# Kernel tuning notes

Hardware: AMD Instinct MI355X
Metric: run time of the kernel (lower is better)

The kernel has to match this reference:

```python
import jax, jax.numpy as jnp
import numpy as np

NUM_HEADS = 12

def setup_inputs() -> dict:
    key = jax.random.key(0)
    ks = jax.random.split(key, 6)
    B, N, C, P = 16, 785, 768, 48
    return {
        "x": jax.random.normal(ks[0], (B, N, C), jnp.float32),
        "qkv_w": jax.random.normal(ks[1], (3 * C, C), jnp.float32) * 0.02,
        "pos_emb": jax.random.normal(ks[2], (N, N, P), jnp.float32) * 0.02,
        "pos_proj_w": jax.random.normal(ks[3], (NUM_HEADS, P), jnp.float32) * 0.02,
        "proj_w": jax.random.normal(ks[4], (C, C), jnp.float32) * 0.02,
        "proj_b": jnp.zeros((C,), jnp.float32),
    }

def reference(x, qkv_w, pos_emb, pos_proj_w, proj_w, proj_b):
    B, N, C = x.shape
    H = NUM_HEADS
    hd = C // H
    scale = hd ** -0.5
    # qkv projection: [B,N,3C] -> q,k,v each [B,H,N,hd]
    qkv = (x @ qkv_w.T).reshape(B, N, 3, H, hd)
    qkv = jnp.transpose(qkv, (2, 0, 3, 1, 4))
    q, k, v = qkv[0], qkv[1], qkv[2]
    # learned relative-position bias: [H,N,N]
    pos_score = jnp.einsum('nmp,hp->hnm', pos_emb, pos_proj_w)
    # attention scores: scale applied AFTER adding bias (matches original)
    attn = (jnp.einsum('bhnd,bhmd->bhnm', q, k) + pos_score[None]) * scale
    attn = jax.nn.softmax(attn, axis=-1)
    out = jnp.einsum('bhnm,bhmd->bhnd', attn, v)
    out = jnp.transpose(out, (0, 2, 1, 3)).reshape(B, N, C)
    return out @ proj_w.T + proj_b
```

## Files before the change

kernel.cpp:

```cpp
#include <hip/hip_runtime.h>
#include <hip/hip_fp16.h>

#define B_ 16
#define N_ 785
#define NP 800
#define C_ 768
#define H_ 12
#define HD_ 64
#define P_ 48
#define M_ (B_*N_)
#define MP_ (B_*NP)
#define POSW 832
#define VTW  832
#define SLOG2E 0.1803368801111244f

#define OFF_Q   0
#define OFF_K   9646080
#define OFF_VT  19292160
#define OFF_POS 29515776
#define OFF_XF  37353216
#define OFF_AO  OFF_XF
#define OFF_WQ  47085312
#define OFF_WP  48854784

struct __align__(16) Half8 { __half h[8]; };
typedef _Float16 half8_t __attribute__((ext_vector_type(8)));
typedef _Float16 half4_t __attribute__((ext_vector_type(4)));
typedef float f32x4 __attribute__((ext_vector_type(4)));

__device__ __forceinline__ void gl16(const void* g, void* l) {
    __builtin_amdgcn_global_load_lds(
        (const __attribute__((address_space(1))) void*)g,
        (__attribute__((address_space(3))) void*)l, 16, 0, 0);
}

__device__ __forceinline__ int xcd_swz(int o, int nwg) {
    const int q = nwg >> 3, r = nwg & 7;
    const int xcd = o & 7, idx = o >> 3;
    const int base = xcd < r ? xcd * (q + 1) : r * (q + 1) + (xcd - r) * q;
    return base + idx;
}

#define NX4 2411520
#define NQ4 442368
#define NP4 147456
#define NTOT4 (NX4+NQ4+NP4)

__global__ __launch_bounds__(256) void convert_f16(
    const float* __restrict__ x, const float* __restrict__ wq,
    const float* __restrict__ wp, _Float16* __restrict__ xo,
    _Float16* __restrict__ wqo, _Float16* __restrict__ wpo)
{
    int i = blockIdx.x * 256 + threadIdx.x;
    const float4* s; _Float16* d; int o;
    if (i < NX4)            { s = (const float4*)x;  d = xo;  o = i; }
    else if (i < NX4 + NQ4) { s = (const float4*)wq; d = wqo; o = i - NX4; }
    else                    { s = (const float4*)wp; d = wpo; o = i - NX4 - NQ4; }
    float4 v = s[o];
    half4_t h = { (_Float16)v.x, (_Float16)v.y, (_Float16)v.z, (_Float16)v.w };
    *(half4_t*)&d[o * 4] = h;
}

#define QKV_NWG (18 * 100)

__global__ __launch_bounds__(256) void qkv_gemm_mfma(
    const _Float16* __restrict__ A, const _Float16* __restrict__ Bw,
    _Float16* __restrict__ qh, _Float16* __restrict__ kh, _Float16* __restrict__ vth)
{
    __shared__ _Float16 Asl[2][128 * 32];
    __shared__ _Float16 Bsl[2][128 * 32];

    const int t  = threadIdx.x;
    const int w  = t >> 6;
    const int l  = t & 63;
    const int lr = l & 15;
    const int lg = l >> 4;
    const int wm = (w >> 1) * 64;
    const int wn = (w & 1) * 64;

    const int g   = xcd_swz(blockIdx.x, QKV_NWG);
    const int nt  = g % 18;
    const int n0  = nt * 128;
    const int mp0 = (g / 18) * 128;
    const int tsel  = nt / 6;
    const bool isV  = (tsel == 2);
    const int nbase = n0 - tsel * 768;

    const int f1 = t + 256;
    const int ar0 = t >> 2,  ac0 = (t & 3) * 8;
    const int ar1 = f1 >> 2, ac1 = (f1 & 3) * 8;
    const int mpa = mp0 + ar0, mpb = mp0 + ar1;
    const int xra = (mpa / NP) * N_ + min(mpa % NP, N_ - 1);
    const int xrb = (mpb / NP) * N_ + min(mpb % NP, N_ - 1);
    const _Float16* Ag0 = A  + (size_t)xra * 768 + ac0;
    const _Float16* Ag1 = A  + (size_t)xrb * 768 + ac1;
    const _Float16* Bg0 = Bw + (size_t)(n0 + ar0) * 768 + ac0;
    const _Float16* Bg1 = Bw + (size_t)(n0 + ar1) * 768 + ac1;

    f32x4 acc[4][4];
    #pragma unroll
    for (int i = 0; i < 4; ++i)
        #pragma unroll
        for (int j = 0; j < 4; ++j) acc[i][j] = (f32x4){0.f, 0.f, 0.f, 0.f};

    gl16(Ag0, &Asl[0][t * 8]); gl16(Ag1, &Asl[0][f1 * 8]);
    gl16(Bg0, &Bsl[0][t * 8]); gl16(Bg1, &Bsl[0][f1 * 8]);
    __syncthreads();

    #pragma unroll 2
    for (int it = 0; it < 24; ++it) {
        const int cur = it & 1;
        if (it < 23) {
            const int kn = (it + 1) * 32;
            gl16(Ag0 + kn, &Asl[cur ^ 1][t * 8]); gl16(Ag1 + kn, &Asl[cur ^ 1][f1 * 8]);
            gl16(Bg0 + kn, &Bsl[cur ^ 1][t * 8]); gl16(Bg1 + kn, &Bsl[cur ^ 1][f1 * 8]);
        }
        half8_t af[4], bf[4];
        #pragma unroll
        for (int i = 0; i < 4; ++i)
            af[i] = *(const half8_t*)&Asl[cur][(wm + i * 16 + lr) * 32 + lg * 8];
        #pragma unroll
        for (int j = 0; j < 4; ++j)
            bf[j] = *(const half8_t*)&Bsl[cur][(wn + j * 16 + lr) * 32 + lg * 8];
        __builtin_amdgcn_s_setprio(1);
        if (!isV) {
            #pragma unroll
            for (int i = 0; i < 4; ++i)
                #pragma unroll
                for (int j = 0; j < 4; ++j)
                    acc[i][j] = __builtin_amdgcn_mfma_f32_16x16x32_f16(bf[j], af[i], acc[i][j], 0, 0, 0);
        } else {
            #pragma unroll
            for (int i = 0; i < 4; ++i)
                #pragma unroll
                for (int j = 0; j < 4; ++j)
                    acc[i][j] = __builtin_amdgcn_mfma_f32_16x16x32_f16(af[i], bf[j], acc[i][j], 0, 0, 0);
        }
        __builtin_amdgcn_s_setprio(0);
        __syncthreads();
    }

    if (!isV) {
        _Float16* dstb = (tsel == 0) ? qh : kh;
        const float sc  = (tsel == 0) ? SLOG2E : 1.0f;
        #pragma unroll
        for (int i = 0; i < 4; ++i) {
            const int mp = mp0 + wm + i * 16 + lr;
            const int bb = mp / NP;
            const int nn = mp - bb * NP;
            if (nn >= N_) continue;
            #pragma unroll
            for (int j = 0; j < 4; ++j) {
                const int nq = nbase + wn + j * 16 + lg * 4;
                const int hh = nq >> 6, dd = nq & 63;
                half4_t hv = { (_Float16)(acc[i][j][0] * sc), (_Float16)(acc[i][j][1] * sc),
                               (_Float16)(acc[i][j][2] * sc), (_Float16)(acc[i][j][3] * sc) };
                *(half4_t*)(dstb + ((size_t)(bb * H_ + hh) * N_ + nn) * HD_ + dd) = hv;
            }
        }
    } else {
        #pragma unroll
        for (int i = 0; i < 4; ++i) {
            const int mq  = mp0 + wm + i * 16 + lg * 4;
            const int bb  = mq / NP;
            const int nn0 = mq - bb * NP;
            if (nn0 >= N_) continue;
            const bool full = (nn0 + 3) < N_;
            #pragma unroll
            for (int j = 0; j < 4; ++j) {
                const int n  = nbase + wn + j * 16 + lr;
                const int hh = n >> 6, dd = n & 63;
                _Float16* vb = vth + ((size_t)(bb * H_ + hh) * HD_ + dd) * VTW;
                if (full) {
                    half4_t hv = { (_Float16)acc[i][j][0], (_Float16)acc[i][j][1],
                                   (_Float16)acc[i][j][2], (_Float16)acc[i][j][3] };
                    *(half4_t*)(vb + nn0) = hv;
                } else {
                    #pragma unroll
                    for (int r = 0; r < 4; ++r)
                        if (nn0 + r < N_) vb[nn0 + r] = (_Float16)acc[i][j][r];
                }
            }
        }
    }
}

__global__ __launch_bounds__(256) void pos_kernel(
    const float* __restrict__ pe, const float* __restrict__ pw,
    __half* __restrict__ posh)
{
    __shared__ float W[H_][P_];
    const int t = threadIdx.x;
    for (int i = t; i < H_ * P_; i += 256) W[i / P_][i % P_] = pw[i];
    __syncthreads();
    int nm = blockIdx.x * 256 + t;
    if (nm >= N_ * N_) return;
    float e[48];
    const float4* src = (const float4*)(pe + (size_t)nm * 48);
    #pragma unroll
    for (int i = 0; i < 12; ++i) {
        float4 v = src[i];
        e[4*i] = v.x; e[4*i+1] = v.y; e[4*i+2] = v.z; e[4*i+3] = v.w;
    }
    int n = nm / N_, m = nm - n * N_;
    #pragma unroll
    for (int hh = 0; hh < H_; ++hh) {
        float s = 0.f;
        #pragma unroll
        for (int p = 0; p < 48; ++p) s = fmaf(e[p], W[hh][p], s);
        posh[((size_t)hh * N_ + n) * POSW + m] = __float2half(s * SLOG2E);
    }
}

#define NQT 13
#define ATT_NWG (192 * NQT)

__global__ __launch_bounds__(256) void attn_mfma(
    const _Float16* __restrict__ qh, const _Float16* __restrict__ kh,
    const _Float16* __restrict__ vt, const _Float16* __restrict__ posh,
    _Float16* __restrict__ aoh)
{
    __shared__ _Float16 Kl[64][72];
    __shared__ _Float16 Vl[64][72];

    const int t  = threadIdx.x;
    const int w  = t >> 6;
    const int l  = t & 63;
    const int lr = l & 15;
    const int lg = l >> 4;

    const int g2   = xcd_swz(blockIdx.x, ATT_NWG);
    const int qt   = g2 % NQT;
    const int rest = g2 / NQT;
    const int b    = rest & 15;
    const int h    = rest >> 4;
    const int bh   = b * H_ + h;
    const int n0   = qt * 64;

    const int qrow = n0 + w * 16 + lr;
    const int qrc  = qrow < N_ ? qrow : N_ - 1;
    const _Float16* qbase = qh + ((size_t)bh * N_ + qrc) * HD_;
    const half8_t qf0 = *(const half8_t*)(qbase + lg * 8);
    const half8_t qf1 = *(const half8_t*)(qbase + 32 + lg * 8);

    f32x4 O0 = {0.f,0.f,0.f,0.f}, O1 = O0, O2 = O0, O3 = O0;
    float m_run = -1e30f;
    float l_lane = 0.f;

    const int srow = t >> 2;
    const int scol = (t & 3) * 16;
    const _Float16* kRow = kh + ((size_t)bh * N_) * HD_ + scol;
    const _Float16* vRow = vt + ((size_t)bh * HD_ + srow) * VTW + scol;
    const _Float16* bFrag = posh + ((size_t)h * N_ + qrc) * POSW + lg * 4;

    half8_t rk0, rk1, rv0, rv1;
    half4_t rbc[4], rbn[4];
    {
        const int gm = srow < N_ ? srow : N_ - 1;
        const half8_t* ks = (const half8_t*)(kRow + (size_t)gm * HD_);
        rk0 = ks[0]; rk1 = ks[1];
        const half8_t* vs = (const half8_t*)vRow;
        rv0 = vs[0]; rv1 = vs[1];
        #pragma unroll
        for (int ms = 0; ms < 4; ++ms)
            rbc[ms] = *(const half4_t*)(bFrag + ms * 16);
    }

    for (int c = 0; c < 13; ++c) {
        *(half8_t*)&Kl[srow][scol]     = rk0;
        *(half8_t*)&Kl[srow][scol + 8] = rk1;
        *(half8_t*)&Vl[srow][scol]     = rv0;
        *(half8_t*)&Vl[srow][scol + 8] = rv1;
        __syncthreads();

        if (c < 12) {
            const int m0n = (c + 1) * 64;
            const int gm  = (m0n + srow) < N_ ? (m0n + srow) : N_ - 1;
            const half8_t* ks = (const half8_t*)(kRow + (size_t)gm * HD_);
            rk0 = ks[0]; rk1 = ks[1];
            const half8_t* vs = (const half8_t*)(vRow + m0n);
            rv0 = vs[0]; rv1 = vs[1];
            #pragma unroll
            for (int ms = 0; ms < 4; ++ms)
                rbn[ms] = *(const half4_t*)(bFrag + m0n + ms * 16);
        }

        f32x4 s[4];
        __builtin_amdgcn_s_setprio(1);
        #pragma unroll
        for (int ms = 0; ms < 4; ++ms) {
            f32x4 acc = { (float)rbc[ms][0], (float)rbc[ms][1],
                          (float)rbc[ms][2], (float)rbc[ms][3] };
            half8_t k0 = *(const half8_t*)&Kl[ms * 16 + lr][lg * 8];
            half8_t k1 = *(const half8_t*)&Kl[ms * 16 + lr][32 + lg * 8];
            acc = __builtin_amdgcn_mfma_f32_16x16x32_f16(k0, qf0, acc, 0, 0, 0);
            acc = __builtin_amdgcn_mfma_f32_16x16x32_f16(k1, qf1, acc, 0, 0, 0);
            s[ms] = acc;
        }
        __builtin_amdgcn_s_setprio(0);

        if (c == 12) {
            #pragma unroll
            for (int ms = 0; ms < 4; ++ms)
                #pragma unroll
                for (int r = 0; r < 4; ++r)
                    if (ms * 16 + lg * 4 + r >= 17) s[ms][r] = -1e30f;
        }

        float x0 = fmaxf(fmaxf(s[0][0], s[0][1]), s[0][2]);
        float x1 = fmaxf(fmaxf(s[0][3], s[1][0]), s[1][1]);
        float x2 = fmaxf(fmaxf(s[1][2], s[1][3]), s[2][0]);
        float x3 = fmaxf(fmaxf(s[2][1], s[2][2]), s[2][3]);
        float x4 = fmaxf(fmaxf(s[3][0], s[3][1]), s[3][2]);
        float smax = fmaxf(fmaxf(fmaxf(x0, x1), x2),
                           fmaxf(fmaxf(x3, x4), s[3][3]));
        smax = fmaxf(smax, __shfl_xor(smax, 16));
        smax = fmaxf(smax, __shfl_xor(smax, 32));

        if (__any(smax > m_run + 8.f)) {
            const float mn    = fmaxf(m_run, smax);
            const float alpha = exp2f(m_run - mn);
            m_run = mn;
            l_lane *= alpha;
            const float a0 = __shfl(alpha, lg * 4 + 0);
            const float a1 = __shfl(alpha, lg * 4 + 1);
            const float a2 = __shfl(alpha, lg * 4 + 2);
            const float a3 = __shfl(alpha, lg * 4 + 3);
            O0[0]*=a0; O0[1]*=a1; O0[2]*=a2; O0[3]*=a3;
            O1[0]*=a0; O1[1]*=a1; O1[2]*=a2; O1[3]*=a3;
            O2[0]*=a0; O2[1]*=a1; O2[2]*=a2; O2[3]*=a3;
            O3[0]*=a0; O3[1]*=a1; O3[2]*=a2; O3[3]*=a3;
        }

        float p[4][4];
        float psum = 0.f;
        #pragma unroll
        for (int ms = 0; ms < 4; ++ms)
            #pragma unroll
            for (int r = 0; r < 4; ++r) {
                p[ms][r] = exp2f(s[ms][r] - m_run);
                psum += p[ms][r];
            }
        l_lane += psum;

        half8_t pa0 = { (_Float16)p[0][0], (_Float16)p[0][1], (_Float16)p[0][2], (_Float16)p[0][3],
                        (_Float16)p[1][0], (_Float16)p[1][1], (_Float16)p[1][2], (_Float16)p[1][3] };
        half8_t pa1 = { (_Float16)p[2][0], (_Float16)p[2][1], (_Float16)p[2][2], (_Float16)p[2][3],
                        (_Float16)p[3][0], (_Float16)p[3][1], (_Float16)p[3][2], (_Float16)p[3][3] };

        __builtin_amdgcn_s_setprio(1);
        #pragma unroll
        for (int ds = 0; ds < 4; ++ds) {
            const _Float16* vr = &Vl[ds * 16 + lr][0];
            half4_t v00 = *(const half4_t*)&vr[lg * 4];
            half4_t v01 = *(const half4_t*)&vr[16 + lg * 4];
            half4_t v10 = *(const half4_t*)&vr[32 + lg * 4];
            half4_t v11 = *(const half4_t*)&vr[48 + lg * 4];
            half8_t vf0 = __builtin_shufflevector(v00, v01, 0, 1, 2, 3, 4, 5, 6, 7);
            half8_t vf1 = __builtin_shufflevector(v10, v11, 0, 1, 2, 3, 4, 5, 6, 7);
            f32x4& Od = (ds == 0 ? O0 : ds == 1 ? O1 : ds == 2 ? O2 : O3);
            Od = __builtin_amdgcn_mfma_f32_16x16x32_f16(pa0, vf0, Od, 0, 0, 0);
            Od = __builtin_amdgcn_mfma_f32_16x16x32_f16(pa1, vf1, Od, 0, 0, 0);
        }
        __builtin_amdgcn_s_setprio(0);
        __syncthreads();

        #pragma unroll
        for (int ms = 0; ms < 4; ++ms) rbc[ms] = rbn[ms];
    }

    float l_row = l_lane;
    l_row += __shfl_xor(l_row, 16);
    l_row += __shfl_xor(l_row, 32);
    const int bb = bh / H_;
    #pragma unroll
    for (int r = 0; r < 4; ++r) {
        const int n = n0 + w * 16 + lg * 4 + r;
        if (n >= N_) continue;
        const float lv  = __shfl(l_row, lg * 4 + r);
        const float inv = 1.f / lv;
        _Float16* dst = aoh + ((size_t)(bb * N_ + n)) * C_ + h * HD_;
        dst[0 * 16 + lr] = (_Float16)(O0[r] * inv);
        dst[1 * 16 + lr] = (_Float16)(O1[r] * inv);
        dst[2 * 16 + lr] = (_Float16)(O2[r] * inv);
        dst[3 * 16 + lr] = (_Float16)(O3[r] * inv);
    }
}

#define PROJ_NWG (6 * 99)

__global__ __launch_bounds__(256) void proj_gemm_mfma(
    const _Float16* __restrict__ A, const _Float16* __restrict__ Bw,
    const float* __restrict__ bias, float* __restrict__ out)
{
    __shared__ _Float16 Asl[2][128 * 32];
    __shared__ _Float16 Bsl[2][128 * 32];

    const int t  = threadIdx.x;
    const int w  = t >> 6;
    const int l  = t & 63;
    const int lr = l & 15;
    const int lg = l >> 4;
    const int wm = (w >> 1) * 64;
    const int wn = (w & 1) * 64;

    const int g  = xcd_swz(blockIdx.x, PROJ_NWG);
    const int n0 = (g % 6) * 128;
    const int m0 = (g / 6) * 128;

    const int f1 = t + 256;
    const int ar0 = t >> 2,  ac0 = (t & 3) * 8;
    const int ar1 = f1 >> 2, ac1 = (f1 & 3) * 8;
    const int ma0 = min(m0 + ar0, M_ - 1);
    const int ma1 = min(m0 + ar1, M_ - 1);
    const _Float16* Ag0 = A  + (size_t)ma0 * 768 + ac0;
    const _Float16* Ag1 = A  + (size_t)ma1 * 768 + ac1;
    const _Float16* Bg0 = Bw + (size_t)(n0 + ar0) * 768 + ac0;
    const _Float16* Bg1 = Bw + (size_t)(n0 + ar1) * 768 + ac1;

    f32x4 acc[4][4];
    #pragma unroll
    for (int i = 0; i < 4; ++i)
        #pragma unroll
        for (int j = 0; j < 4; ++j) acc[i][j] = (f32x4){0.f, 0.f, 0.f, 0.f};

    gl16(Ag0, &Asl[0][t * 8]); gl16(Ag1, &Asl[0][f1 * 8]);
    gl16(Bg0, &Bsl[0][t * 8]); gl16(Bg1, &Bsl[0][f1 * 8]);
    __syncthreads();

    #pragma unroll 2
    for (int it = 0; it < 24; ++it) {
        const int cur = it & 1;
        if (it < 23) {
            const int kn = (it + 1) * 32;
            gl16(Ag0 + kn, &Asl[cur ^ 1][t * 8]); gl16(Ag1 + kn, &Asl[cur ^ 1][f1 * 8]);
            gl16(Bg0 + kn, &Bsl[cur ^ 1][t * 8]); gl16(Bg1 + kn, &Bsl[cur ^ 1][f1 * 8]);
        }
        half8_t af[4], bf[4];
        #pragma unroll
        for (int i = 0; i < 4; ++i)
            af[i] = *(const half8_t*)&Asl[cur][(wm + i * 16 + lr) * 32 + lg * 8];
        #pragma unroll
        for (int j = 0; j < 4; ++j)
            bf[j] = *(const half8_t*)&Bsl[cur][(wn + j * 16 + lr) * 32 + lg * 8];
        __builtin_amdgcn_s_setprio(1);
        #pragma unroll
        for (int i = 0; i < 4; ++i)
            #pragma unroll
            for (int j = 0; j < 4; ++j)
                acc[i][j] = __builtin_amdgcn_mfma_f32_16x16x32_f16(bf[j], af[i], acc[i][j], 0, 0, 0);
        __builtin_amdgcn_s_setprio(0);
        __syncthreads();
    }

    float4 bj4[4];
    #pragma unroll
    for (int j = 0; j < 4; ++j)
        bj4[j] = *(const float4*)&bias[n0 + wn + j * 16 + lg * 4];
    #pragma unroll
    for (int i = 0; i < 4; ++i) {
        const int m = m0 + wm + i * 16 + lr;
        if (m >= M_) continue;
        #pragma unroll
        for (int j = 0; j < 4; ++j) {
            const int nq = n0 + wn + j * 16 + lg * 4;
            float4 o = { acc[i][j][0] + bj4[j].x, acc[i][j][1] + bj4[j].y,
                         acc[i][j][2] + bj4[j].z, acc[i][j][3] + bj4[j].w };
            *(float4*)&out[(size_t)m * 768 + nq] = o;
        }
    }
}

extern "C" void kernel_launch(void* const* d_in, const int* in_sizes, int n_in,
                              void* d_out, int out_size, void* d_ws, size_t ws_size,
                              hipStream_t stream)
{
    const float* x     = (const float*)d_in[0];
    const float* qkv_w = (const float*)d_in[1];
    const float* pe    = (const float*)d_in[2];
    const float* pw    = (const float*)d_in[3];
    const float* pjw   = (const float*)d_in[4];
    const float* pjb   = (const float*)d_in[5];
    float* out = (float*)d_out;

    _Float16* wsh  = (_Float16*)d_ws;
    _Float16* qh   = wsh + OFF_Q;
    _Float16* kh   = wsh + OFF_K;
    _Float16* vth  = wsh + OFF_VT;
    _Float16* posh = wsh + OFF_POS;
    _Float16* xf   = wsh + OFF_XF;
    _Float16* aoh  = wsh + OFF_AO;
    _Float16* wqf  = wsh + OFF_WQ;
    _Float16* wpf  = wsh + OFF_WP;

    convert_f16<<<dim3(NTOT4 / 256), 256, 0, stream>>>(x, qkv_w, pjw, xf, wqf, wpf);
    qkv_gemm_mfma<<<dim3(QKV_NWG), 256, 0, stream>>>(xf, wqf, qh, kh, vth);
    pos_kernel<<<dim3((N_ * N_ + 255) / 256), 256, 0, stream>>>(pe, pw, (__half*)posh);
    attn_mfma<<<dim3(ATT_NWG), 256, 0, stream>>>(qh, kh, vth, posh, aoh);
    proj_gemm_mfma<<<dim3(PROJ_NWG), 256, 0, stream>>>(aoh, wpf, pjb, out);
}
```

Before: 263.5 us.

## Double-buffer K/V LDS tiles and compute softmax row sums via MFMA

Makes the K and V shared-memory tiles double-buffered, so the next chunk is written to the alternate buffer after the PV MFMAs. This removes one of the two block barriers per iteration. V is permuted on store so each lane reads its B fragment with a single 8-wide LDS load instead of two 4-wide loads plus a shuffle. The softmax denominator is accumulated by an extra pair of MFMAs against a vector of ones, replacing scalar adds and the final cross-lane reductions. The max reduction shuffles now run only when a rescale is triggered. Costs are doubled LDS usage, which may lower occupancy, and two extra MFMAs per chunk.

New measurement: 261.6 us. About the same (-0.7%).

```diff
diff --git a/kernel.cpp b/kernel.cpp
--- a/kernel.cpp
+++ b/kernel.cpp
@@ -220,12 +220,12 @@
     const _Float16* __restrict__ vt, const _Float16* __restrict__ posh,
     _Float16* __restrict__ aoh)
 {
-    __shared__ _Float16 Kl[64][72];
-    __shared__ _Float16 Vl[64][72];
+    __shared__ _Float16 Kl[2][64][72];
+    __shared__ _Float16 Vl[2][64][72];
 
     const int t  = threadIdx.x;
+    const int l  = t & 63;
     const int w  = t >> 6;
-    const int l  = t & 63;
     const int lr = l & 15;
     const int lg = l >> 4;
 
@@ -244,11 +244,15 @@
     const half8_t qf1 = *(const half8_t*)(qbase + 32 + lg * 8);
 
     f32x4 O0 = {0.f,0.f,0.f,0.f}, O1 = O0, O2 = O0, O3 = O0;
+    f32x4 lacc = {0.f,0.f,0.f,0.f};
     float m_run = -1e30f;
-    float l_lane = 0.f;
+
+    const half8_t vones = { (_Float16)1.f, (_Float16)1.f, (_Float16)1.f, (_Float16)1.f,
+                            (_Float16)1.f, (_Float16)1.f, (_Float16)1.f, (_Float16)1.f };
 
     const int srow = t >> 2;
     const int scol = (t & 3) * 16;
+    const int vbase = (scol & 32) + ((scol & 16) >> 2);
     const _Float16* kRow = kh + ((size_t)bh * N_) * HD_ + scol;
     const _Float16* vRow = vt + ((size_t)bh * HD_ + srow) * VTW + scol;
     const _Float16* bFrag = posh + ((size_t)h * N_ + qrc) * POSW + lg * 4;
@@ -265,12 +269,18 @@
         for (int ms = 0; ms < 4; ++ms)
             rbc[ms] = *(const half4_t*)(bFrag + ms * 16);
     }
+    *(half8_t*)&Kl[0][srow][scol]     = rk0;
+    *(half8_t*)&Kl[0][srow][scol + 8] = rk1;
+    {
+        _Float16* vd = &Vl[0][srow][vbase];
+        *(half4_t*)(vd +  0) = __builtin_shufflevector(rv0, rv0, 0, 1, 2, 3);
+        *(half4_t*)(vd +  8) = __builtin_shufflevector(rv0, rv0, 4, 5, 6, 7);
+        *(half4_t*)(vd + 16) = __builtin_shufflevector(rv1, rv1, 0, 1, 2, 3);
+        *(half4_t*)(vd + 24) = __builtin_shufflevector(rv1, rv1, 4, 5, 6, 7);
+    }
 
     for (int c = 0; c < 13; ++c) {
-        *(half8_t*)&Kl[srow][scol]     = rk0;
-        *(half8_t*)&Kl[srow][scol + 8] = rk1;
-        *(half8_t*)&Vl[srow][scol]     = rv0;
-        *(half8_t*)&Vl[srow][scol + 8] = rv1;
+        const int cur = c & 1;
         __syncthreads();
 
         if (c < 12) {
@@ -291,8 +301,8 @@
         for (int ms = 0; ms < 4; ++ms) {
             f32x4 acc = { (float)rbc[ms][0], (float)rbc[ms][1],
                           (float)rbc[ms][2], (float)rbc[ms][3] };
-            half8_t k0 = *(const half8_t*)&Kl[ms * 16 + lr][lg * 8];
-            half8_t k1 = *(const half8_t*)&Kl[ms * 16 + lr][32 + lg * 8];
+            half8_t k0 = *(const half8_t*)&Kl[cur][ms * 16 + lr][lg * 8];
+            half8_t k1 = *(const half8_t*)&Kl[cur][ms * 16 + lr][32 + lg * 8];
             acc = __builtin_amdgcn_mfma_f32_16x16x32_f16(k0, qf0, acc, 0, 0, 0);
             acc = __builtin_amdgcn_mfma_f32_16x16x32_f16(k1, qf1, acc, 0, 0, 0);
             s[ms] = acc;
@@ -312,16 +322,15 @@
         float x2 = fmaxf(fmaxf(s[1][2], s[1][3]), s[2][0]);
         float x3 = fmaxf(fmaxf(s[2][1], s[2][2]), s[2][3]);
         float x4 = fmaxf(fmaxf(s[3][0], s[3][1]), s[3][2]);
-        float smax = fmaxf(fmaxf(fmaxf(x0, x1), x2),
-                           fmaxf(fmaxf(x3, x4), s[3][3]));
-        smax = fmaxf(smax, __shfl_xor(smax, 16));
-        smax = fmaxf(smax, __shfl_xor(smax, 32));
-
-        if (__any(smax > m_run + 8.f)) {
-            const float mn    = fmaxf(m_run, smax);
+        float mq = fmaxf(fmaxf(fmaxf(x0, x1), x2),
+                         fmaxf(fmaxf(x3, x4), s[3][3]));
+
+        if (__any(mq > m_run + 8.f)) {
+            float v = fmaxf(mq, __shfl_xor(mq, 16));
+            v = fmaxf(v, __shfl_xor(v, 32));
+            const float mn    = fmaxf(m_run, v);
             const float alpha = exp2f(m_run - mn);
             m_run = mn;
-            l_lane *= alpha;
             const float a0 = __shfl(alpha, lg * 4 + 0);
             const float a1 = __shfl(alpha, lg * 4 + 1);
             const float a2 = __shfl(alpha, lg * 4 + 2);
@@ -330,18 +339,15 @@
             O1[0]*=a0; O1[1]*=a1; O1[2]*=a2; O1[3]*=a3;
             O2[0]*=a0; O2[1]*=a1; O2[2]*=a2; O2[3]*=a3;
             O3[0]*=a0; O3[1]*=a1; O3[2]*=a2; O3[3]*=a3;
+            lacc[0]*=a0; lacc[1]*=a1; lacc[2]*=a2; lacc[3]*=a3;
         }
 
         float p[4][4];
-        float psum = 0.f;
         #pragma unroll
         for (int ms = 0; ms < 4; ++ms)
             #pragma unroll
-            for (int r = 0; r < 4; ++r) {
+            for (int r = 0; r < 4; ++r)
                 p[ms][r] = exp2f(s[ms][r] - m_run);
-                psum += p[ms][r];
-            }
-        l_lane += psum;
 
         half8_t pa0 = { (_Float16)p[0][0], (_Float16)p[0][1], (_Float16)p[0][2], (_Float16)p[0][3],
                         (_Float16)p[1][0], (_Float16)p[1][1], (_Float16)p[1][2], (_Float16)p[1][3] };
@@ -349,36 +355,39 @@
                         (_Float16)p[3][0], (_Float16)p[3][1], (_Float16)p[3][2], (_Float16)p[3][3] };
 
         __builtin_amdgcn_s_setprio(1);
+        lacc = __builtin_amdgcn_mfma_f32_16x16x32_f16(pa0, vones, lacc, 0, 0, 0);
+        lacc = __builtin_amdgcn_mfma_f32_16x16x32_f16(pa1, vones, lacc, 0, 0, 0);
         #pragma unroll
         for (int ds = 0; ds < 4; ++ds) {
-            const _Float16* vr = &Vl[ds * 16 + lr][0];
-            half4_t v00 = *(const half4_t*)&vr[lg * 4];
-            half4_t v01 = *(const half4_t*)&vr[16 + lg * 4];
-            half4_t v10 = *(const half4_t*)&vr[32 + lg * 4];
-            half4_t v11 = *(const half4_t*)&vr[48 + lg * 4];
-            half8_t vf0 = __builtin_shufflevector(v00, v01, 0, 1, 2, 3, 4, 5, 6, 7);
-            half8_t vf1 = __builtin_shufflevector(v10, v11, 0, 1, 2, 3, 4, 5, 6, 7);
+            const _Float16* vr = &Vl[cur][ds * 16 + lr][0];
+            half8_t vf0 = *(const half8_t*)&vr[lg * 8];
+            half8_t vf1 = *(const half8_t*)&vr[32 + lg * 8];
             f32x4& Od = (ds == 0 ? O0 : ds == 1 ? O1 : ds == 2 ? O2 : O3);
             Od = __builtin_amdgcn_mfma_f32_16x16x32_f16(pa0, vf0, Od, 0, 0, 0);
             Od = __builtin_amdgcn_mfma_f32_16x16x32_f16(pa1, vf1, Od, 0, 0, 0);
         }
         __builtin_amdgcn_s_setprio(0);
-        __syncthreads();
-
-        #pragma unroll
-        for (int ms = 0; ms < 4; ++ms) rbc[ms] = rbn[ms];
-    }
-
-    float l_row = l_lane;
-    l_row += __shfl_xor(l_row, 16);
-    l_row += __shfl_xor(l_row, 32);
+
+        if (c < 12) {
+            const int nxt = cur ^ 1;
+            *(half8_t*)&Kl[nxt][srow][scol]     = rk0;
+            *(half8_t*)&Kl[nxt][srow][scol + 8] = rk1;
+            _Float16* vd = &Vl[nxt][srow][vbase];
+            *(half4_t*)(vd +  0) = __builtin_shufflevector(rv0, rv0, 0, 1, 2, 3);
+            *(half4_t*)(vd +  8) = __builtin_shufflevector(rv0, rv0, 4, 5, 6, 7);
+            *(half4_t*)(vd + 16) = __builtin_shufflevector(rv1, rv1, 0, 1, 2, 3);
+            *(half4_t*)(vd + 24) = __builtin_shufflevector(rv1, rv1, 4, 5, 6, 7);
+            #pragma unroll
+            for (int ms = 0; ms < 4; ++ms) rbc[ms] = rbn[ms];
+        }
+    }
+
     const int bb = bh / H_;
     #pragma unroll
     for (int r = 0; r < 4; ++r) {
         const int n = n0 + w * 16 + lg * 4 + r;
         if (n >= N_) continue;
-        const float lv  = __shfl(l_row, lg * 4 + r);
-        const float inv = 1.f / lv;
+        const float inv = 1.f / lacc[r];
         _Float16* dst = aoh + ((size_t)(bb * N_ + n)) * C_ + h * HD_;
         dst[0 * 16 + lr] = (_Float16)(O0[r] * inv);
         dst[1 * 16 + lr] = (_Float16)(O1[r] * inv);
```
